# Performance work log

Measured on AMD Instinct MI355X. Metric: run time of the kernel, lower is better.

The kernel has to match this reference:

```python
import jax, jax.numpy as jnp
import numpy as np

T, B, H, L = 512, 64, 512, 2  # seq_len, batch, hidden(=input), layers


def setup_inputs() -> dict:
    key = jax.random.key(0)
    k0, k1, k2 = jax.random.split(key, 3)
    x = jax.random.normal(k0, (T, B, H), jnp.float32)
    # weights stored as [L, in, 4H] so the per-step op is inp @ W
    Wh = jax.random.normal(k1, (L, H, 4 * H), jnp.float32) * 0.02
    Wx = jax.random.normal(k2, (L, H, 4 * H), jnp.float32) * 0.02
    bh = jnp.zeros((L, 4 * H), jnp.float32)  # only hidden_lin has bias
    return {"x": x, "Wh": Wh, "Wx": Wx, "bh": bh}


def reference(x, Wh, Wx, bh):
    n_layers, H4 = bh.shape
    Hd = H4 // 4
    Bd = x.shape[1]
    h0 = jnp.zeros((n_layers, Bd, Hd), x.dtype)
    c0 = jnp.zeros_like(h0)

    def step(carry, xt):
        h, c = carry  # each [L, B, H]
        inp = xt
        hs, cs = [], []
        for l in range(n_layers):  # small fixed layer count
            ifgo = inp @ Wx[l] + h[l] @ Wh[l] + bh[l]  # [B, 4H]
            i, f, g, o = jnp.split(ifgo, 4, axis=-1)
            c_next = jax.nn.sigmoid(f) * c[l] + jax.nn.sigmoid(i) * jnp.tanh(g)
            h_next = jax.nn.sigmoid(o) * jnp.tanh(c_next)
            hs.append(h_next)
            cs.append(c_next)
            inp = h_next
        h_new = jnp.stack(hs)
        c_new = jnp.stack(cs)
        return (h_new, c_new), h_new[-1]

    (h_fin, c_fin), out = jax.lax.scan(step, (h0, c0), x)  # out: [T, B, H]
    return out, h_fin, c_fin
```

## Files before the change

kernel.cpp:

```cpp
#include <hip/hip_runtime.h>
#include <hip/hip_bf16.h>


#define TSEQ 512
#define BATCH 64
#define HID 512
#define H4 2048
#define BH (BATCH * HID)
#define DEPTH 8
#define QR 16
#define NSTRIP 16
#define RPR 256

typedef short bf16x8 __attribute__((ext_vector_type(8)));
typedef float f32x4 __attribute__((ext_vector_type(4)));
typedef float f32x2 __attribute__((ext_vector_type(2)));
typedef unsigned long long u64;
typedef u64 u64x2 __attribute__((ext_vector_type(2)));

__device__ __forceinline__ ushort f32_to_bf16(float f) {
    unsigned u = __builtin_bit_cast(unsigned, f);
    u += 0x7FFFu + ((u >> 16) & 1u);
    return (ushort)(u >> 16);
}

__device__ __forceinline__ float tanh_fast(float x) {
    return 1.f - 2.f / (1.f + __expf(2.f * x));
}

__device__ __forceinline__ bf16x8 load_tagged(const u64* p, unsigned tag) {
    u64x2 a, b;
    for (;;) {
        asm volatile("global_load_dwordx4 %0, %2, off sc1\n\t"
                     "global_load_dwordx4 %1, %3, off sc1\n\t"
                     "s_waitcnt vmcnt(0)"
                     : "=&v"(a), "=&v"(b) : "v"(p), "v"(p + 2) : "memory");
        if ((unsigned)(a.x >> 32) == tag && (unsigned)(a.y >> 32) == tag &&
            (unsigned)(b.x >> 32) == tag && (unsigned)(b.y >> 32) == tag) break;
        __builtin_amdgcn_s_sleep(1);
    }
    union { unsigned u[4]; bf16x8 v; } r;
    r.u[0] = (unsigned)a.x; r.u[1] = (unsigned)a.y;
    r.u[2] = (unsigned)b.x; r.u[3] = (unsigned)b.y;
    return r.v;
}

__global__ __launch_bounds__(256) void convert_x(const float* __restrict__ x,
                                                 ushort* __restrict__ xq) {
    const int n4 = (TSEQ * BATCH * HID) / 4;
    int stride = gridDim.x * blockDim.x;
    for (int i = blockIdx.x * blockDim.x + threadIdx.x; i < n4; i += stride) {
        float4 v = ((const float4*)x)[i];
        ushort4 o;
        o.x = f32_to_bf16(v.x);
        o.y = f32_to_bf16(v.y);
        o.z = f32_to_bf16(v.z);
        o.w = f32_to_bf16(v.w);
        ((ushort4*)xq)[i] = o;
    }
}

__global__ __launch_bounds__(256) void transpose_w(const float* __restrict__ Wh,
                                                   const float* __restrict__ Wx,
                                                   ushort* __restrict__ WT) {
    int bid = blockIdx.x;
    int m  = bid >> 8;
    int kt = (bid >> 5) & 7;
    int nt = bid & 31;
    const float* src = ((m & 1) ? Wh : Wx) + (size_t)(m >> 1) * (HID * H4);

    __shared__ float tile[64][65];
    int c  = threadIdx.x & 63;
    int r0 = (threadIdx.x >> 6) * 16;
    for (int i = 0; i < 16; ++i) {
        int r = r0 + i;
        tile[r][c] = src[(size_t)(kt * 64 + r) * H4 + nt * 64 + c];
    }
    __syncthreads();
    int k  = threadIdx.x & 63;
    int n0 = (threadIdx.x >> 6) * 16;
    for (int i = 0; i < 16; ++i) {
        int n = n0 + i;
        WT[(size_t)m * (H4 * HID) + (size_t)(nt * 64 + n) * HID + kt * 64 + k] =
            f32_to_bf16(tile[k][n]);
    }
}

__global__ __launch_bounds__(1024, 4) void lstm_persistent(
    const ushort* __restrict__ WT,
    const ushort* __restrict__ xq,
    const float*  __restrict__ bh,
    u64*   __restrict__ h0T,
    u64*   __restrict__ h1T,
    float* __restrict__ out,
    int*   __restrict__ f1prog)
{
    const int wg    = blockIdx.x;
    const int layer = wg >> 6;
    const int quad  = (wg >> 4) & 3;
    const int strip = wg & 15;
    const int j0    = strip * 32;
    const int tid   = threadIdx.x;
    const int wave  = tid >> 6;
    const int lane  = tid & 63;
    const int g     = wave & 3;
    const int ch    = (wave >> 2) & 1;
    const int kh    = wave >> 3;
    const int lo    = lane & 15;
    const int hi    = lane >> 4;

    int* myprog = &f1prog[quad * NSTRIP + strip];

    const ushort* bx = WT + (size_t)(layer * 2 + 0) * (H4 * HID)
                     + (size_t)(g * 512 + j0 + ch * 16 + lo) * HID + kh * 256 + hi * 8;
    const ushort* bw = WT + (size_t)(layer * 2 + 1) * (H4 * HID)
                     + (size_t)(g * 512 + j0 + ch * 16 + lo) * HID + kh * 256 + hi * 8;
    bf16x8 wx[8], wh[8];
#pragma unroll
    for (int kk = 0; kk < 8; ++kk) {
        wx[kk] = *(const bf16x8*)(bx + kk * 32);
        wh[kk] = *(const bf16x8*)(bw + kk * 32);
    }
#pragma unroll
    for (int kk = 0; kk < 8; ++kk) {
        asm volatile("" : "+v"(wx[kk]));
        asm volatile("" : "+v"(wh[kk]));
    }

    const int grow = tid >> 4;
    const int cp   = (tid & 15) * 2;
    f32x2 bias2[4];
#pragma unroll
    for (int gg = 0; gg < 4; ++gg)
        bias2[gg] = *(const f32x2*)&bh[layer * H4 + gg * 512 + j0 + cp];
    f32x2 creg = (f32x2)(0.f);

    __shared__ __align__(16) ushort ldsA[2][QR * HID];
    __shared__ __align__(16) float  lds_g[4][2][QR][34];

    const int row  = tid >> 6;
    const int kba  = tid & 63;
    const int goff  = (quad * QR + row) * HID + kba * 8;
    const int roff  = (quad * QR + row) * RPR + kba * 4;
    const int laddr = ((row << 10) + (kba << 4)) ^ ((row & 15) << 4);
    const bf16x8 zero8 = {0, 0, 0, 0, 0, 0, 0, 0};

    for (int s = 0; s <= TSEQ; ++s) {
        const int t = s - layer;
        const bool active = (t >= 0 && t < TSEQ);

        if (active) {
            bf16x8 v0, v1;
            if (layer == 0) {
                v0 = *(const bf16x8*)(xq + (size_t)t * BH + goff);
                if (s >= 6 && tid < NSTRIP) {
                    const int* f = &f1prog[quad * NSTRIP + tid];
                    while (__hip_atomic_load(f, __ATOMIC_RELAXED,
                                             __HIP_MEMORY_SCOPE_AGENT) < s - 6)
                        __builtin_amdgcn_s_sleep(1);
                }
                v1 = (t == 0) ? zero8
                              : load_tagged(h0T + (size_t)((t - 1) & 7) * (BATCH * RPR)
                                            + roff, (unsigned)t);
            } else {
                v0 = load_tagged(h0T + (size_t)(t & 7) * (BATCH * RPR) + roff,
                                 (unsigned)(t + 1));
                v1 = (t == 0) ? zero8
                              : load_tagged(h1T + (size_t)((t - 1) & 7) * (BATCH * RPR)
                                            + roff, (unsigned)t);
            }
            __builtin_amdgcn_sched_barrier(0);
            *(bf16x8*)((char*)&ldsA[0][0] + laddr) = v0;
            *(bf16x8*)((char*)&ldsA[1][0] + laddr) = v1;
            __syncthreads();

            if (layer == 1 && tid == 0)
                __hip_atomic_store(myprog, s, __ATOMIC_RELAXED,
                                   __HIP_MEMORY_SCOPE_AGENT);

            f32x4 acc0 = (f32x4)(0.f), acc1 = (f32x4)(0.f);
#pragma unroll
            for (int kk = 0; kk < 8; ++kk) {
                const int kb2 = kh * 512 + kk * 64 + hi * 16;
                const int ad  = ((lo << 10) + kb2) ^ ((lo & 15) << 4);
                bf16x8 a1 = *(const bf16x8*)((char*)&ldsA[0][0] + ad);
                bf16x8 a2 = *(const bf16x8*)((char*)&ldsA[1][0] + ad);
                acc0 = __builtin_amdgcn_mfma_f32_16x16x32_bf16(a1, wx[kk], acc0, 0, 0, 0);
                acc1 = __builtin_amdgcn_mfma_f32_16x16x32_bf16(a2, wh[kk], acc1, 0, 0, 0);
            }
            f32x4 acc = acc0 + acc1;
#pragma unroll
            for (int r = 0; r < 4; ++r)
                lds_g[g][kh][hi * 4 + r][ch * 16 + lo] = acc[r];
            __syncthreads();

            if (tid < 256) {
                f32x2 gi = *(const f32x2*)&lds_g[0][0][grow][cp]
                         + *(const f32x2*)&lds_g[0][1][grow][cp] + bias2[0];
                f32x2 gf = *(const f32x2*)&lds_g[1][0][grow][cp]
                         + *(const f32x2*)&lds_g[1][1][grow][cp] + bias2[1];
                f32x2 gg = *(const f32x2*)&lds_g[2][0][grow][cp]
                         + *(const f32x2*)&lds_g[2][1][grow][cp] + bias2[2];
                f32x2 go = *(const f32x2*)&lds_g[3][0][grow][cp]
                         + *(const f32x2*)&lds_g[3][1][grow][cp] + bias2[3];
                f32x2 cn, hn;
#pragma unroll
                for (int q = 0; q < 2; ++q) {
                    float si = 1.f / (1.f + __expf(-gi[q]));
                    float sf = 1.f / (1.f + __expf(-gf[q]));
                    float so = 1.f / (1.f + __expf(-go[q]));
                    float tg = tanh_fast(gg[q]);
                    cn[q] = sf * creg[q] + si * tg;
                    hn[q] = so * tanh_fast(cn[q]);
                }
                creg = cn;

                unsigned hp = (unsigned)f32_to_bf16(hn[0])
                            | ((unsigned)f32_to_bf16(hn[1]) << 16);
                u64 rec = (u64)hp | ((u64)(unsigned)(t + 1) << 32);
                u64* hw = ((layer == 0) ? h0T : h1T)
                        + (size_t)(t & 7) * (BATCH * RPR)
                        + (size_t)(quad * QR + grow) * RPR + ((j0 + cp) >> 1);
                __hip_atomic_store(hw, rec, __ATOMIC_RELAXED,
                                   __HIP_MEMORY_SCOPE_AGENT);

                const int hoff = (quad * QR + grow) * HID + j0 + cp;
                if (layer == 1)
                    *(f32x2*)&out[(size_t)t * BH + hoff] = hn;
                if (t == TSEQ - 1) {
                    size_t base = (size_t)TSEQ * BH + (size_t)layer * BH + hoff;
                    *(f32x2*)&out[base] = hn;
                    *(f32x2*)&out[base + 2 * (size_t)BH] = cn;
                }
            }
        } else {
            if (layer == 1 && tid == 0)
                __hip_atomic_store(myprog, s, __ATOMIC_RELAXED,
                                   __HIP_MEMORY_SCOPE_AGENT);
            __syncthreads();
        }
    }
}

extern "C" void kernel_launch(void* const* d_in, const int* in_sizes, int n_in,
                              void* d_out, int out_size, void* d_ws, size_t ws_size,
                              hipStream_t stream) {
    const float* x  = (const float*)d_in[0];
    const float* Wh = (const float*)d_in[1];
    const float* Wx = (const float*)d_in[2];
    const float* bh = (const float*)d_in[3];
    float* out = (float*)d_out;

    char* ws = (char*)d_ws;
    ushort* WT = (ushort*)ws;
    ushort* xq = (ushort*)(ws + ((size_t)8 << 20));
    char* state = ws + ((size_t)8 << 20) + ((size_t)32 << 20);
    u64* h0T = (u64*)state;
    u64* h1T = h0T + (size_t)DEPTH * BATCH * RPR;
    int* f1prog = (int*)(h1T + (size_t)DEPTH * BATCH * RPR);
    size_t clear_bytes = (size_t)2 * DEPTH * BATCH * RPR * sizeof(u64)
                       + 64 * sizeof(int);

    hipMemsetAsync(state, 0, clear_bytes, stream);
    convert_x<<<2048, 256, 0, stream>>>(x, xq);
    transpose_w<<<1024, 256, 0, stream>>>(Wh, Wx, WT);
    lstm_persistent<<<128, 1024, 0, stream>>>(WT, xq, bh, h0T, h1T, out, f1prog);
}
```

Before: 1.650 ms.

## Split the LDS staging loads across dedicated wave groups per operand

Each thread used to load both operands (input and recurrent h) with its own tagged spin-poll. Now threads 512+ fetch only the recurrent h strip with wider loads, threads 256-511 fetch only the input or layer-0 h strip, and threads 0-255 only handle the progress wait. Separating the operands lets the two spin-polls run in parallel on different waves and uses fewer, wider per-thread requests. The cost is that fewer threads issue loads, so the latency of a single thread's poll could lengthen the critical path.

```diff
diff --git a/kernel.cpp b/kernel.cpp
--- a/kernel.cpp
+++ b/kernel.cpp
@@ -11,6 +11,7 @@
 #define QR 16
 #define NSTRIP 16
 #define RPR 256
+#define BRPR (BATCH * RPR)
 
 typedef short bf16x8 __attribute__((ext_vector_type(8)));
 typedef float f32x4 __attribute__((ext_vector_type(4)));
@@ -28,21 +29,15 @@
     return 1.f - 2.f / (1.f + __expf(2.f * x));
 }
 
-__device__ __forceinline__ bf16x8 load_tagged(const u64* p, unsigned tag) {
-    u64x2 a, b;
-    for (;;) {
-        asm volatile("global_load_dwordx4 %0, %2, off sc1\n\t"
-                     "global_load_dwordx4 %1, %3, off sc1\n\t"
-                     "s_waitcnt vmcnt(0)"
-                     : "=&v"(a), "=&v"(b) : "v"(p), "v"(p + 2) : "memory");
-        if ((unsigned)(a.x >> 32) == tag && (unsigned)(a.y >> 32) == tag &&
-            (unsigned)(b.x >> 32) == tag && (unsigned)(b.y >> 32) == tag) break;
-        __builtin_amdgcn_s_sleep(1);
-    }
+__device__ __forceinline__ bf16x8 unpack_recs(u64x2 a, u64x2 b) {
     union { unsigned u[4]; bf16x8 v; } r;
     r.u[0] = (unsigned)a.x; r.u[1] = (unsigned)a.y;
     r.u[2] = (unsigned)b.x; r.u[3] = (unsigned)b.y;
     return r.v;
+}
+__device__ __forceinline__ bool tags4(u64x2 a, u64x2 b, unsigned tag) {
+    return (unsigned)(a.x >> 32) == tag && (unsigned)(a.y >> 32) == tag &&
+           (unsigned)(b.x >> 32) == tag && (unsigned)(b.y >> 32) == tag;
 }
 
 __global__ __launch_bounds__(256) void convert_x(const float* __restrict__ x,
@@ -138,11 +133,22 @@
     __shared__ __align__(16) ushort ldsA[2][QR * HID];
     __shared__ __align__(16) float  lds_g[4][2][QR][34];
 
-    const int row  = tid >> 6;
-    const int kba  = tid & 63;
-    const int goff  = (quad * QR + row) * HID + kba * 8;
-    const int roff  = (quad * QR + row) * RPR + kba * 4;
-    const int laddr = ((row << 10) + (kba << 4)) ^ ((row & 15) << 4);
+    const int sj   = tid - 512;
+    const int srow = (sj >> 5) & 15;
+    const int scs  = sj & 31;
+    const int roffS = (quad * QR + srow) * RPR + scs * 8;
+    const int lS0 = (srow << 10) + (((scs * 2 + 0) << 4) ^ ((srow & 15) << 4));
+    const int lS1 = (srow << 10) + (((scs * 2 + 1) << 4) ^ ((srow & 15) << 4));
+    const int cj   = tid - 256;
+    const int crow = (cj >> 4) & 15;
+    const int ccs  = cj & 15;
+    const int roffC = (quad * QR + crow) * RPR + ccs * 16;
+    const int goffC = (quad * QR + crow) * HID + ccs * 32;
+    int lC[4];
+#pragma unroll
+    for (int k = 0; k < 4; ++k)
+        lC[k] = (crow << 10) + (((ccs * 4 + k) << 4) ^ ((crow & 15) << 4));
+
     const bf16x8 zero8 = {0, 0, 0, 0, 0, 0, 0, 0};
 
     for (int s = 0; s <= TSEQ; ++s) {
@@ -150,28 +156,82 @@
         const bool active = (t >= 0 && t < TSEQ);
 
         if (active) {
-            bf16x8 v0, v1;
-            if (layer == 0) {
-                v0 = *(const bf16x8*)(xq + (size_t)t * BH + goff);
-                if (s >= 6 && tid < NSTRIP) {
+            if (tid >= 512) {
+                bf16x8 w0, w1;
+                const bool selfzero = layer ? (s == 1) : (s == 0);
+                if (selfzero) {
+                    w0 = zero8; w1 = zero8;
+                } else {
+                    const u64* p = (layer ? h1T : h0T)
+                        + (size_t)((layer ? (s - 2) : (s - 1)) & 7) * BRPR + roffS;
+                    const unsigned tag = (unsigned)(layer ? (s - 1) : s);
+                    u64x2 a, b, c, d;
+                    for (;;) {
+                        asm volatile(
+                            "global_load_dwordx4 %0, %4, off sc1\n\t"
+                            "global_load_dwordx4 %1, %5, off sc1\n\t"
+                            "global_load_dwordx4 %2, %6, off sc1\n\t"
+                            "global_load_dwordx4 %3, %7, off sc1\n\t"
+                            "s_waitcnt vmcnt(0)"
+                            : "=&v"(a), "=&v"(b), "=&v"(c), "=&v"(d)
+                            : "v"(p), "v"(p + 2), "v"(p + 4), "v"(p + 6) : "memory");
+                        if (tags4(a, b, tag) && tags4(c, d, tag)) break;
+                        __builtin_amdgcn_s_sleep(1);
+                    }
+                    w0 = unpack_recs(a, b);
+                    w1 = unpack_recs(c, d);
+                }
+                *(bf16x8*)((char*)&ldsA[1][0] + lS0) = w0;
+                *(bf16x8*)((char*)&ldsA[1][0] + lS1) = w1;
+            } else if (tid >= 256) {
+                bf16x8 u0, u1, u2, u3;
+                if (layer == 0) {
+                    const ushort* X = xq + (size_t)t * BH + goffC;
+                    u0 = *(const bf16x8*)(X + 0);
+                    u1 = *(const bf16x8*)(X + 8);
+                    u2 = *(const bf16x8*)(X + 16);
+                    u3 = *(const bf16x8*)(X + 24);
+                } else {
+                    const u64* p = h0T + (size_t)((s - 1) & 7) * BRPR + roffC;
+                    const unsigned tag = (unsigned)s;
+                    u64x2 a, b, c, d, e, f, g2, h2;
+                    for (;;) {
+                        asm volatile(
+                            "global_load_dwordx4 %0, %8, off sc1\n\t"
+                            "global_load_dwordx4 %1, %9, off sc1\n\t"
+                            "global_load_dwordx4 %2, %10, off sc1\n\t"
+                            "global_load_dwordx4 %3, %11, off sc1\n\t"
+                            "global_load_dwordx4 %4, %12, off sc1\n\t"
+                            "global_load_dwordx4 %5, %13, off sc1\n\t"
+                            "global_load_dwordx4 %6, %14, off sc1\n\t"
+                            "global_load_dwordx4 %7, %15, off sc1\n\t"
+                            "s_waitcnt vmcnt(0)"
+                            : "=&v"(a), "=&v"(b), "=&v"(c), "=&v"(d),
+                              "=&v"(e), "=&v"(f), "=&v"(g2), "=&v"(h2)
+                            : "v"(p), "v"(p + 2), "v"(p + 4), "v"(p + 6),
+                              "v"(p + 8), "v"(p + 10), "v"(p + 12), "v"(p + 14)
+                            : "memory");
+                        if (tags4(a, b, tag) && tags4(c, d, tag) &&
+                            tags4(e, f, tag) && tags4(g2, h2, tag)) break;
+                        __builtin_amdgcn_s_sleep(1);
+                    }
+                    u0 = unpack_recs(a, b);
+                    u1 = unpack_recs(c, d);
+                    u2 = unpack_recs(e, f);
+                    u3 = unpack_recs(g2, h2);
+                }
+                *(bf16x8*)((char*)&ldsA[0][0] + lC[0]) = u0;
+                *(bf16x8*)((char*)&ldsA[0][0] + lC[1]) = u1;
+                *(bf16x8*)((char*)&ldsA[0][0] + lC[2]) = u2;
+                *(bf16x8*)((char*)&ldsA[0][0] + lC[3]) = u3;
+            } else {
+                if (layer == 0 && s >= 6 && tid < NSTRIP) {
                     const int* f = &f1prog[quad * NSTRIP + tid];
                     while (__hip_atomic_load(f, __ATOMIC_RELAXED,
                                              __HIP_MEMORY_SCOPE_AGENT) < s - 6)
                         __builtin_amdgcn_s_sleep(1);
                 }
-                v1 = (t == 0) ? zero8
-                              : load_tagged(h0T + (size_t)((t - 1) & 7) * (BATCH * RPR)
-                                            + roff, (unsigned)t);
-            } else {
-                v0 = load_tagged(h0T + (size_t)(t & 7) * (BATCH * RPR) + roff,
-                                 (unsigned)(t + 1));
-                v1 = (t == 0) ? zero8
-                              : load_tagged(h1T + (size_t)((t - 1) & 7) * (BATCH * RPR)
-                                            + roff, (unsigned)t);
             }
-            __builtin_amdgcn_sched_barrier(0);
-            *(bf16x8*)((char*)&ldsA[0][0] + laddr) = v0;
-            *(bf16x8*)((char*)&ldsA[1][0] + laddr) = v1;
             __syncthreads();
 
             if (layer == 1 && tid == 0)
@@ -219,7 +279,7 @@
                             | ((unsigned)f32_to_bf16(hn[1]) << 16);
                 u64 rec = (u64)hp | ((u64)(unsigned)(t + 1) << 32);
                 u64* hw = ((layer == 0) ? h0T : h1T)
-                        + (size_t)(t & 7) * (BATCH * RPR)
+                        + (size_t)(t & 7) * BRPR
                         + (size_t)(quad * QR + grow) * RPR + ((j0 + cp) >> 1);
                 __hip_atomic_store(hw, rec, __ATOMIC_RELAXED,
                                    __HIP_MEMORY_SCOPE_AGENT);
@@ -256,9 +316,9 @@
     ushort* xq = (ushort*)(ws + ((size_t)8 << 20));
     char* state = ws + ((size_t)8 << 20) + ((size_t)32 << 20);
     u64* h0T = (u64*)state;
-    u64* h1T = h0T + (size_t)DEPTH * BATCH * RPR;
-    int* f1prog = (int*)(h1T + (size_t)DEPTH * BATCH * RPR);
-    size_t clear_bytes = (size_t)2 * DEPTH * BATCH * RPR * sizeof(u64)
+    u64* h1T = h0T + (size_t)DEPTH * BRPR;
+    int* f1prog = (int*)(h1T + (size_t)DEPTH * BRPR);
+    size_t clear_bytes = (size_t)2 * DEPTH * BRPR * sizeof(u64)
                        + 64 * sizeof(int);
 
     hipMemsetAsync(state, 0, clear_bytes, stream);
```

Measured after the change: 3.674 ms. +122.7%, slower.
